# Performance work log

Hardware: AMD Instinct MI355X
Metric: run time of the kernel (lower is better)

## Reference

```python
import jax, jax.numpy as jnp
import numpy as np

WINDOWS = (3, 5, 7)
B, L, D = 8, 512, 768
NUM_LABELS = 9


def setup_inputs() -> dict:
    key = jax.random.key(0)
    ks = jax.random.split(key, 7)
    n = len(WINDOWS)
    return {
        "sequence_output": jax.random.normal(ks[0], (B, L, D), jnp.float32),
        "W_ih": jax.random.normal(ks[1], (n, 4 * D, D), jnp.float32) * 0.02,
        "W_hh": jax.random.normal(ks[2], (n, 4 * D, D), jnp.float32) * 0.02,
        "b_ih": jax.random.normal(ks[3], (n, 4 * D), jnp.float32) * 0.02,
        "b_hh": jax.random.normal(ks[4], (n, 4 * D), jnp.float32) * 0.02,
        "lin_w": jax.random.normal(ks[5], (NUM_LABELS, D), jnp.float32) * 0.02,
        "lin_b": jnp.zeros((NUM_LABELS,), jnp.float32),
    }


def _windowed_lstm(x, w, Wih, Whh, bih, bhh):
    # Vectorized equivalent of windows_sequence: for each position i, run an
    # LSTM over the sorted in-range neighborhood of radius w//2 around i and
    # take the final hidden state (state after the rightmost valid token).
    Bb, Ll, Dd = x.shape
    h = w // 2
    offs = jnp.arange(-h, h + 1)                      # [W]
    pos = jnp.arange(Ll)[:, None] + offs[None, :]     # [L, W]
    valid = (pos >= 0) & (pos < Ll)                   # [L, W]
    idx = jnp.clip(pos, 0, Ll - 1)
    win = x[:, idx, :]                                # [B, L, W, D]
    xs = jnp.moveaxis(win, 2, 0)                      # [W, B, L, D] scan axis first
    vs = valid.T                                      # [W, L]

    def step(carry, inp):
        hs, cs = carry                                # [B, L, D] each
        x_t, v_t = inp                                # [B, L, D], [L]
        gates = x_t @ Wih.T + bih + hs @ Whh.T + bhh  # [B, L, 4D]; torch gate order i,f,g,o
        i, f, g, o = jnp.split(gates, 4, axis=-1)
        i = jax.nn.sigmoid(i)
        f = jax.nn.sigmoid(f)
        g = jnp.tanh(g)
        o = jax.nn.sigmoid(o)
        c_new = f * cs + i * g
        h_new = o * jnp.tanh(c_new)
        m = v_t[None, :, None]                        # skip out-of-range window slots
        return (jnp.where(m, h_new, hs), jnp.where(m, c_new, cs)), None

    init = (jnp.zeros_like(x), jnp.zeros_like(x))
    (h_fin, _), _ = jax.lax.scan(step, init, (xs, vs))
    return h_fin                                      # [B, L, D]


def reference(sequence_output, W_ih, W_hh, b_ih, b_hh, lin_w, lin_b):
    x = sequence_output
    # one short LSTM scan per window size (small fixed set)
    locals_ = jnp.stack(
        [_windowed_lstm(x, w, W_ih[k], W_hh[k], b_ih[k], b_hh[k])
         for k, w in enumerate(WINDOWS)], axis=2)     # [B, L, n_win, D]
    d_k = x.shape[-1]
    attn = jnp.einsum('bld,blnd->bln', x, locals_) / jnp.sqrt(jnp.float32(d_k))
    attn = jax.nn.softmax(attn, axis=-1)
    local_features = jnp.einsum('bln,blnd->bld', attn, locals_)
    out = x + local_features
    return out @ lin_w.T + lin_b                      # [B, L, num_labels]
```

## Files before the change

kernel.cpp:

```cpp
#include <hip/hip_runtime.h>
#include <math.h>

#define BB   8
#define LL   512
#define DD   768
#define G4   3072
#define NW   3
#define NLAB 9
#define MM   4096

typedef unsigned short u16;
typedef __attribute__((ext_vector_type(8))) __bf16 bf16x8;
typedef __attribute__((ext_vector_type(4))) float  f32x4;

#define AS1 __attribute__((address_space(1)))
#define AS3 __attribute__((address_space(3)))

#define OFF_G    ((size_t)0)
#define OFF_C    ((size_t)75497472)
#define OFF_H    ((size_t)113246208)
#define OFF_XB   ((size_t)150994944)
#define OFF_WIHB ((size_t)157286400)
#define OFF_WHHB ((size_t)171442176)

#if __has_builtin(__builtin_amdgcn_exp2f)
#define FEXP2(x) __builtin_amdgcn_exp2f(x)
#else
#define FEXP2(x) exp2f(x)
#endif
#if __has_builtin(__builtin_amdgcn_rcpf)
#define FRCP(x) __builtin_amdgcn_rcpf(x)
#else
#define FRCP(x) (1.0f / (x))
#endif
#define LOG2E  1.4426950408889634f
#define LOG2E2 2.8853900817779268f

__device__ __forceinline__ float sigm(float x) {
    return FRCP(1.0f + FEXP2(-LOG2E * x));
}
__device__ __forceinline__ float ftanh(float x) {
    return 1.0f - 2.0f * FRCP(1.0f + FEXP2(LOG2E2 * x));
}

__device__ __forceinline__ u16 f2bf(float f) {
    union { float f; unsigned u; } v; v.f = f;
    unsigned r = v.u + 0x7FFFu + ((v.u >> 16) & 1u);
    return (u16)(r >> 16);
}
__device__ __forceinline__ float bf2f(u16 h) {
    union { unsigned u; float f; } v; v.u = ((unsigned)h) << 16;
    return v.f;
}

__global__ __launch_bounds__(256)
void k_cvt3(const float* __restrict__ a, const float* __restrict__ b,
            const float* __restrict__ c,
            u16* __restrict__ oa, u16* __restrict__ ob, u16* __restrict__ oc,
            int na4, int nb4, int nc4)
{
    int i = blockIdx.x * 256 + threadIdx.x;
    const float* src; u16* dst; int j;
    if (i < na4)                  { src = a; dst = oa; j = i; }
    else if (i < na4 + nb4)       { src = b; dst = ob; j = i - na4; }
    else if (i < na4 + nb4 + nc4) { src = c; dst = oc; j = i - na4 - nb4; }
    else return;
    float4 v = reinterpret_cast<const float4*>(src)[j];
    ushort4 o;
    o.x = f2bf(v.x); o.y = f2bf(v.y); o.z = f2bf(v.z); o.w = f2bf(v.w);
    reinterpret_cast<ushort4*>(dst)[j] = o;
}

template<int MODE>
__global__ __launch_bounds__(512, 2)
void k_mfma(const u16* __restrict__ Ab,
            const u16* __restrict__ Wb,
            const float* __restrict__ bih,
            const float* __restrict__ bhh,
            u16* __restrict__ Gp,
            u16* __restrict__ hnext,
            float* __restrict__ cbuf,
            int kmin, int s)
{
    const int k = kmin + blockIdx.z;

    const int f  = blockIdx.y * 16 + blockIdx.x;
    const int c  = f & 7;
    const int j_ = f >> 3;
    const int bx = (c & 3) * 4 + (j_ & 3);
    const int by = (c >> 2) * 6 + (j_ >> 2);
    const int r0 = bx * 256;
    const int n0 = by * 64;

    const int tid  = threadIdx.x;
    const int lane = tid & 63;
    const int wid  = tid >> 6;
    const int wm   = wid >> 2;
    const int wn   = wid & 3;

    __shared__ bf16x8 As[2][2048];
    __shared__ bf16x8 Bs[2][2048];

    const u16* Asrc = (MODE == 0) ? Ab : (Ab + (size_t)k * MM * DD);
    const u16* Wk   = Wb + (size_t)k * G4 * DD;

    const int sg = (tid & 7) ^ ((tid >> 3) & 7);
    const u16* gA[4]; const u16* gB[4];
#pragma unroll
    for (int i = 0; i < 4; ++i) {
        int rowA = i * 64 + (tid >> 3);
        gA[i] = Asrc + (size_t)(r0 + rowA) * DD + sg * 8;
        int p    = rowA;
        int g    = (p >> 4) & 3;
        int cell = (p & 15) + 16 * (p >> 6);
        int j    = g * DD + n0 + cell;
        gB[i] = Wk + (size_t)j * DD + sg * 8;
    }

    auto stage = [&](int buf, int k0) {
#pragma unroll
        for (int i = 0; i < 4; ++i) {
            __builtin_amdgcn_global_load_lds(
                (const AS1 void*)(gA[i] + k0),
                (AS3 void*)&As[buf][i * 512 + tid], 16, 0, 0);
            __builtin_amdgcn_global_load_lds(
                (const AS1 void*)(gB[i] + k0),
                (AS3 void*)&Bs[buf][i * 512 + tid], 16, 0, 0);
        }
    };

    f32x4 acc[8][4];
#pragma unroll
    for (int a = 0; a < 8; ++a)
#pragma unroll
        for (int b = 0; b < 4; ++b) acc[a][b] = (f32x4)0.0f;

    const int c15 = lane & 15;
    const int khi = lane >> 4;

    stage(0, 0);

    int cur = 0;
    for (int t = 0; t < 12; ++t) {
        if (t < 11) {
            stage(cur ^ 1, (t + 1) * 64);
            asm volatile("s_waitcnt vmcnt(8)" ::: "memory");
        } else {
            asm volatile("s_waitcnt vmcnt(0)" ::: "memory");
        }
        __builtin_amdgcn_s_barrier();

        __builtin_amdgcn_s_setprio(1);
#pragma unroll
        for (int ks = 0; ks < 2; ++ks) {
            bf16x8 af[8], bfr[4];
#pragma unroll
            for (int mi = 0; mi < 8; ++mi) {
                int row  = wm * 128 + mi * 16 + c15;
                int slot = (ks * 4 + khi) ^ (row & 7);
                af[mi] = As[cur][row * 8 + slot];
            }
#pragma unroll
            for (int ni = 0; ni < 4; ++ni) {
                int row  = wn * 64 + ni * 16 + c15;
                int slot = (ks * 4 + khi) ^ (row & 7);
                bfr[ni] = Bs[cur][row * 8 + slot];
            }
#pragma unroll
            for (int mi = 0; mi < 8; ++mi)
#pragma unroll
                for (int ni = 0; ni < 4; ++ni)
                    acc[mi][ni] = __builtin_amdgcn_mfma_f32_16x16x32_bf16(
                        af[mi], bfr[ni], acc[mi][ni], 0, 0, 0);
        }
        __builtin_amdgcn_s_setprio(0);

        __builtin_amdgcn_s_barrier();
        cur ^= 1;
    }

    const int n  = n0 + 16 * wn + c15;
    const int hw = k + 1;

    if (MODE == 0) {
        u16*   Gk = Gp    + ((size_t)k * MM * DD) * 4;
        u16*   h0 = hnext + (size_t)k * MM * DD;
        float* c0 = cbuf  + (size_t)k * MM * DD;
        const float bs0 = bih[k * G4 + 0 * DD + n] + bhh[k * G4 + 0 * DD + n];
        const float bs1 = bih[k * G4 + 1 * DD + n] + bhh[k * G4 + 1 * DD + n];
        const float bs2 = bih[k * G4 + 2 * DD + n] + bhh[k * G4 + 2 * DD + n];
        const float bs3 = bih[k * G4 + 3 * DD + n] + bhh[k * G4 + 3 * DD + n];
#pragma unroll
        for (int mi = 0; mi < 8; ++mi)
#pragma unroll
            for (int q = 0; q < 4; ++q) {
                int r = r0 + wm * 128 + mi * 16 + khi * 4 + q;
                float p0 = acc[mi][0][q] + bs0;
                float p1 = acc[mi][1][q] + bs1;
                float p2 = acc[mi][2][q] + bs2;
                float p3 = acc[mi][3][q] + bs3;
                ushort4 pk;
                pk.x = f2bf(p0); pk.y = f2bf(p1); pk.z = f2bf(p2); pk.w = f2bf(p3);
                *reinterpret_cast<ushort4*>(Gk + ((size_t)r * DD + n) * 4) = pk;
                int l  = r & (LL - 1);
                bool ok = (l + hw) < LL;
                int rt = ok ? (r + hw) : (r + hw - LL);
                float iv = sigm(p0), gv = ftanh(p2), ov = sigm(p3);
                float cn = iv * gv;
                float hv = ov * ftanh(cn);
                size_t offt = (size_t)rt * DD + n;
                c0[offt] = ok ? cn : 0.0f;
                h0[offt] = ok ? f2bf(hv) : (u16)0;
            }
    } else {
        const u16* Gk = Gp + ((size_t)k * MM * DD) * 4;
        u16*  hn = hnext + (size_t)k * MM * DD;
        const u16* hp = Asrc;
        float* ck = cbuf + (size_t)k * MM * DD;
#pragma unroll
        for (int mi = 0; mi < 8; ++mi)
#pragma unroll
            for (int q = 0; q < 4; ++q) {
                int r = r0 + wm * 128 + mi * 16 + khi * 4 + q;
                int l = r & (LL - 1);
                int pos = l - hw + s;
                bool valid = (pos >= 0) && (pos < LL);
                int posc = min(max(pos, 0), LL - 1);
                ushort4 g4 = *reinterpret_cast<const ushort4*>(
                    Gk + ((size_t)(r - l + posc) * DD + n) * 4);
                float gi = sigm (acc[mi][0][q] + bf2f(g4.x));
                float gf = sigm (acc[mi][1][q] + bf2f(g4.y));
                float gg = ftanh(acc[mi][2][q] + bf2f(g4.z));
                float go = sigm (acc[mi][3][q] + bf2f(g4.w));
                size_t off = (size_t)r * DD + n;
                if (valid) {
                    float cold = ck[off];
                    float cnew = gf * cold + gi * gg;
                    ck[off] = cnew;
                    hn[off] = f2bf(go * ftanh(cnew));
                } else {
                    hn[off] = hp[off];
                }
            }
    }
}

__global__ __launch_bounds__(256)
void k_final(const float* __restrict__ x, const u16* __restrict__ hfin,
             const float* __restrict__ linw, const float* __restrict__ linb,
             float* __restrict__ out)
{
    int wave = threadIdx.x >> 6, lane = threadIdx.x & 63;
    int r = blockIdx.x * 4 + wave;
    const float* xr = x + (size_t)r * DD;
    const u16* h0 = hfin + (size_t)0 * MM * DD + (size_t)r * DD;
    const u16* h1 = hfin + (size_t)1 * MM * DD + (size_t)r * DD;
    const u16* h2 = hfin + (size_t)2 * MM * DD + (size_t)r * DD;

    float xe[12], he0[12], he1[12], he2[12];
    float s0 = 0.f, s1 = 0.f, s2 = 0.f;
#pragma unroll
    for (int q = 0; q < 12; ++q) {
        int e = lane + 64 * q;
        xe[q] = xr[e];
        he0[q] = bf2f(h0[e]); he1[q] = bf2f(h1[e]); he2[q] = bf2f(h2[e]);
        s0 = fmaf(xe[q], he0[q], s0);
        s1 = fmaf(xe[q], he1[q], s1);
        s2 = fmaf(xe[q], he2[q], s2);
    }
#pragma unroll
    for (int d = 1; d < 64; d <<= 1) {
        s0 += __shfl_xor(s0, d, 64);
        s1 += __shfl_xor(s1, d, 64);
        s2 += __shfl_xor(s2, d, 64);
    }
    const float scale = 0.03608439182435161f;
    s0 *= scale; s1 *= scale; s2 *= scale;
    float mx = fmaxf(s0, fmaxf(s1, s2));
    float e0 = FEXP2(LOG2E * (s0 - mx));
    float e1 = FEXP2(LOG2E * (s1 - mx));
    float e2 = FEXP2(LOG2E * (s2 - mx));
    float inv = FRCP(e0 + e1 + e2);
    float a0 = e0 * inv, a1 = e1 * inv, a2 = e2 * inv;

    float p[9];
#pragma unroll
    for (int j = 0; j < 9; ++j) p[j] = 0.0f;
#pragma unroll
    for (int q = 0; q < 12; ++q) {
        int e = lane + 64 * q;
        float o = xe[q] + a0 * he0[q] + a1 * he1[q] + a2 * he2[q];
#pragma unroll
        for (int j = 0; j < 9; ++j)
            p[j] = fmaf(o, linw[j * DD + e], p[j]);
    }
#pragma unroll
    for (int j = 0; j < 9; ++j)
#pragma unroll
        for (int d = 1; d < 64; d <<= 1)
            p[j] += __shfl_xor(p[j], d, 64);
    if (lane == 0) {
#pragma unroll
        for (int j = 0; j < 9; ++j)
            out[(size_t)r * NLAB + j] = p[j] + linb[j];
    }
}

extern "C" void kernel_launch(void* const* d_in, const int* in_sizes, int n_in,
                              void* d_out, int out_size, void* d_ws, size_t ws_size,
                              hipStream_t stream)
{
    const float* x    = (const float*)d_in[0];
    const float* Wih  = (const float*)d_in[1];
    const float* Whh  = (const float*)d_in[2];
    const float* bih  = (const float*)d_in[3];
    const float* bhh  = (const float*)d_in[4];
    const float* linw = (const float*)d_in[5];
    const float* linb = (const float*)d_in[6];
    float* out = (float*)d_out;
    char*  ws  = (char*)d_ws;

    u16*   Gp   = (u16*)  (ws + OFF_G);
    float* C    = (float*)(ws + OFF_C);
    u16*   H    = (u16*)  (ws + OFF_H);
    u16*   xb   = (u16*)  (ws + OFF_XB);
    u16*   Wihb = (u16*)  (ws + OFF_WIHB);
    u16*   Whhb = (u16*)  (ws + OFF_WHHB);

    dim3 blk(256);
    dim3 blkG(512);

    const int na4 = MM * DD / 4;
    const int nb4 = NW * G4 * DD / 4;
    k_cvt3<<<(na4 + 2 * nb4 + 255) / 256, blk, 0, stream>>>(
        x, Wih, Whh, xb, Wihb, Whhb, na4, nb4, nb4);

    k_mfma<0><<<dim3(16, 12, 3), blkG, 0, stream>>>(
        xb, Wihb, bih, bhh, Gp, H, C, 0, 0);

    for (int s = 1; s < 7; ++s) {
        int kmin = (s < 3) ? 0 : ((s < 5) ? 1 : 2);
        int nact = 3 - kmin;
        u16* hprev = H + (size_t)((s - 1) & 1) * NW * MM * DD;
        u16* hnx   = H + (size_t)(s & 1) * NW * MM * DD;
        k_mfma<1><<<dim3(16, 12, nact), blkG, 0, stream>>>(
            hprev, Whhb, nullptr, nullptr, Gp, hnx, C, kmin, s);
    }

    k_final<<<MM / 4, blk, 0, stream>>>(x, H, linw, linb, out);
}
```

Measured before the change: 780.6 us.

## Drop LDS double buffering in MFMA GEMM and raise launch-bounds occupancy

Replaces the two-stage LDS ping-pong, where the next K-tile was prefetched with async global_load_lds while computing on the current one, with a single buffer that loads, syncs, computes, and syncs again each iteration. It also removes the s_setprio hints and raises the launch-bounds minimum blocks per CU from 2 to 4. The aim is to halve LDS use and let more workgroups overlap memory latency across blocks instead of within one block. In exchange, load latency is exposed inside each block and the tighter register budget may cause spills with the 32 accumulator tiles.

```diff
diff --git a/kernel.cpp b/kernel.cpp
--- a/kernel.cpp
+++ b/kernel.cpp
@@ -72,7 +72,7 @@
 }
 
 template<int MODE>
-__global__ __launch_bounds__(512, 2)
+__global__ __launch_bounds__(512, 4)
 void k_mfma(const u16* __restrict__ Ab,
             const u16* __restrict__ Wb,
             const float* __restrict__ bih,
@@ -98,8 +98,8 @@
     const int wm   = wid >> 2;
     const int wn   = wid & 3;
 
-    __shared__ bf16x8 As[2][2048];
-    __shared__ bf16x8 Bs[2][2048];
+    __shared__ bf16x8 As[2048];
+    __shared__ bf16x8 Bs[2048];
 
     const u16* Asrc = (MODE == 0) ? Ab : (Ab + (size_t)k * MM * DD);
     const u16* Wk   = Wb + (size_t)k * G4 * DD;
@@ -117,15 +117,15 @@
         gB[i] = Wk + (size_t)j * DD + sg * 8;
     }
 
-    auto stage = [&](int buf, int k0) {
+    auto stage = [&](int k0) {
 #pragma unroll
         for (int i = 0; i < 4; ++i) {
             __builtin_amdgcn_global_load_lds(
                 (const AS1 void*)(gA[i] + k0),
-                (AS3 void*)&As[buf][i * 512 + tid], 16, 0, 0);
+                (AS3 void*)&As[i * 512 + tid], 16, 0, 0);
             __builtin_amdgcn_global_load_lds(
                 (const AS1 void*)(gB[i] + k0),
-                (AS3 void*)&Bs[buf][i * 512 + tid], 16, 0, 0);
+                (AS3 void*)&Bs[i * 512 + tid], 16, 0, 0);
         }
     };
 
@@ -138,19 +138,9 @@
     const int c15 = lane & 15;
     const int khi = lane >> 4;
 
-    stage(0, 0);
-
-    int cur = 0;
     for (int t = 0; t < 12; ++t) {
-        if (t < 11) {
-            stage(cur ^ 1, (t + 1) * 64);
-            asm volatile("s_waitcnt vmcnt(8)" ::: "memory");
-        } else {
-            asm volatile("s_waitcnt vmcnt(0)" ::: "memory");
-        }
-        __builtin_amdgcn_s_barrier();
-
-        __builtin_amdgcn_s_setprio(1);
+        stage(t * 64);
+        __syncthreads();
 #pragma unroll
         for (int ks = 0; ks < 2; ++ks) {
             bf16x8 af[8], bfr[4];
@@ -158,13 +148,13 @@
             for (int mi = 0; mi < 8; ++mi) {
                 int row  = wm * 128 + mi * 16 + c15;
                 int slot = (ks * 4 + khi) ^ (row & 7);
-                af[mi] = As[cur][row * 8 + slot];
+                af[mi] = As[row * 8 + slot];
             }
 #pragma unroll
             for (int ni = 0; ni < 4; ++ni) {
                 int row  = wn * 64 + ni * 16 + c15;
                 int slot = (ks * 4 + khi) ^ (row & 7);
-                bfr[ni] = Bs[cur][row * 8 + slot];
+                bfr[ni] = Bs[row * 8 + slot];
             }
 #pragma unroll
             for (int mi = 0; mi < 8; ++mi)
@@ -173,10 +163,7 @@
                     acc[mi][ni] = __builtin_amdgcn_mfma_f32_16x16x32_bf16(
                         af[mi], bfr[ni], acc[mi][ni], 0, 0, 0);
         }
-        __builtin_amdgcn_s_setprio(0);
-
-        __builtin_amdgcn_s_barrier();
-        cur ^= 1;
+        __syncthreads();
     }
 
     const int n  = n0 + 16 * wn + c15;
```

Result: slower. 2.319 ms (+197.1%).
